# Optimization experiments

Hardware: AMD Instinct MI355X
Metric: run time of the kernel (lower is better)

## Reference

```python
import jax, jax.numpy as jnp
import numpy as np

HIDDEN = 2048
NUM_HEADS = 32
NUM_KV_HEADS = 8
HEAD_DIM = HIDDEN // NUM_HEADS          # 64
Q_PER_KV = NUM_HEADS // NUM_KV_HEADS    # 4
KV_SIZE = HIDDEN * NUM_KV_HEADS // NUM_HEADS  # 512
BATCH, SEQ = 2, 2048


def setup_inputs() -> dict:
    key = jax.random.key(0)
    ks = jax.random.split(key, 10)
    s = 0.02
    return {
        "x": jax.random.normal(ks[0], (BATCH, SEQ, HIDDEN), jnp.float32),
        "attention_mask": jnp.zeros((BATCH, SEQ), jnp.float32),
        "Wq": jax.random.normal(ks[1], (HIDDEN, HIDDEN), jnp.float32) * s,
        "bq": jnp.zeros((HIDDEN,), jnp.float32),
        "Wk": jax.random.normal(ks[2], (HIDDEN, KV_SIZE), jnp.float32) * s,
        "bk": jnp.zeros((KV_SIZE,), jnp.float32),
        "Wv": jax.random.normal(ks[3], (HIDDEN, KV_SIZE), jnp.float32) * s,
        "bv": jnp.zeros((KV_SIZE,), jnp.float32),
        "Wo": jax.random.normal(ks[4], (HIDDEN, HIDDEN), jnp.float32) * s,
        "bo": jnp.zeros((HIDDEN,), jnp.float32),
    }


def reference(x, attention_mask, Wq, bq, Wk, bk, Wv, bv, Wo, bo):
    b, s, _ = x.shape
    q = x @ Wq + bq                                  # [b,s,H]
    k = x @ Wk + bk                                  # [b,s,kv_size]
    v = x @ Wv + bv
    # q -> [b, kv_heads, q_per_kv, s, head_dim]
    q = q.reshape(b, s, NUM_KV_HEADS, Q_PER_KV, HEAD_DIM).transpose(0, 2, 3, 1, 4)
    # k, v -> [b, kv_heads, s, head_dim]
    k = k.reshape(b, s, NUM_KV_HEADS, HEAD_DIM).transpose(0, 2, 1, 3)
    v = v.reshape(b, s, NUM_KV_HEADS, HEAD_DIM).transpose(0, 2, 1, 3)
    scale = 1.0 / jnp.sqrt(jnp.float32(HEAD_DIM))
    scores = jnp.einsum('bhqsd,bhkd->bhqsk', q, k) * scale   # [b,h,qpk,s,s]
    scores = scores + attention_mask.reshape(b, 1, 1, 1, s)
    attn = jax.nn.softmax(scores, axis=-1)
    out = jnp.einsum('bhqsk,bhkd->bhqsd', attn, v)           # [b,h,qpk,s,d]
    out = out.transpose(0, 3, 1, 2, 4).reshape(b, s, HIDDEN)
    return out @ Wo + bo
```

## Files before the change

### kernel.cpp

```cpp
#include <hip/hip_runtime.h>

typedef __attribute__((ext_vector_type(8))) short short8;
typedef __attribute__((ext_vector_type(4))) float floatx4;
typedef __attribute__((ext_vector_type(4))) unsigned int uintx4;

#define B_ 2
#define S_ 2048
#define H_ 2048
#define LOG2E 1.44269504088896f

#define MFMA(a, b, c) __builtin_amdgcn_mfma_f32_16x16x32_bf16(a, b, c, 0, 0, 0)

__device__ __forceinline__ unsigned short f2bf(float f) {
    unsigned int x = __builtin_bit_cast(unsigned int, f);
    unsigned int r = x + 0x7FFFu + ((x >> 16) & 1u);
    return (unsigned short)(r >> 16);
}

__device__ __forceinline__ void gload_lds16(const unsigned short* g, unsigned short* l) {
    __builtin_amdgcn_global_load_lds(
        (const __attribute__((address_space(1))) void*)g,
        (__attribute__((address_space(3))) void*)l, 16, 0, 0);
}

__global__ __launch_bounds__(256) void conv_f2b(const float* __restrict__ in,
                                                unsigned short* __restrict__ out, int n4,
                                                const float* __restrict__ mask,
                                                float* __restrict__ mw) {
    int i = blockIdx.x * 256 + threadIdx.x;
    if (i < n4) {
        float4 v = ((const float4*)in)[i];
        ushort4 o;
        o.x = f2bf(v.x); o.y = f2bf(v.y); o.z = f2bf(v.z); o.w = f2bf(v.w);
        ((ushort4*)out)[i] = o;
    } else {
        for (int m = threadIdx.x; m < B_ * S_; m += 256)
            mw[m] = mask[m] * LOG2E;
    }
}

__global__ __launch_bounds__(256) void tr_f2b(const float* __restrict__ in,
                                              unsigned short* __restrict__ out,
                                              int R, int C) {
    __shared__ unsigned short t[32][33];
    int c0 = blockIdx.x * 32, r0 = blockIdx.y * 32;
    int tx = threadIdx.x & 31, ty = threadIdx.x >> 5;
#pragma unroll
    for (int i = 0; i < 32; i += 8)
        t[ty + i][tx] = f2bf(in[(size_t)(r0 + ty + i) * C + c0 + tx]);
    __syncthreads();
#pragma unroll
    for (int i = 0; i < 32; i += 8)
        out[(size_t)(c0 + ty + i) * R + r0 + tx] = t[tx][ty + i];
}

__global__ __launch_bounds__(256) void tr_wqkv(const float* __restrict__ Wq,
                                               const float* __restrict__ Wk,
                                               const float* __restrict__ Wv,
                                               unsigned short* __restrict__ WqkvT) {
    __shared__ unsigned short t[32][33];
    int bx = blockIdx.x;
    const float* src; int C, c0, orow;
    if (bx < 64)      { src = Wq; C = 2048; c0 = bx * 32;        orow = bx * 32; }
    else if (bx < 80) { src = Wk; C = 512;  c0 = (bx - 64) * 32; orow = 2048 + (bx - 64) * 32; }
    else              { src = Wv; C = 512;  c0 = (bx - 80) * 32; orow = 2560 + (bx - 80) * 32; }
    int r0 = blockIdx.y * 32;
    int tx = threadIdx.x & 31, ty = threadIdx.x >> 5;
#pragma unroll
    for (int i = 0; i < 32; i += 8)
        t[ty + i][tx] = f2bf(src[(size_t)(r0 + ty + i) * C + c0 + tx]);
    __syncthreads();
#pragma unroll
    for (int i = 0; i < 32; i += 8)
        WqkvT[(size_t)(orow + ty + i) * 2048 + r0 + tx] = t[tx][ty + i];
}

__global__ __launch_bounds__(256) void tr_vperm(const unsigned short* __restrict__ in,
                                                unsigned short* __restrict__ out,
                                                int R, int C, int ipitch,
                                                size_t ibs, size_t obs) {
    __shared__ unsigned short t[32][33];
    in += (size_t)blockIdx.z * ibs; out += (size_t)blockIdx.z * obs;
    int c0 = blockIdx.x * 32, r0 = blockIdx.y * 32;
    int tx = threadIdx.x & 31, ty = threadIdx.x >> 5;
#pragma unroll
    for (int i = 0; i < 32; i += 8)
        t[ty + i][tx] = in[(size_t)(r0 + ty + i) * ipitch + c0 + tx];
    __syncthreads();
    int s = r0 + tx;
    int sl = s & 63;
    int j = sl >> 4, q = (sl >> 2) & 3, ii = sl & 3;
    int sp = (s & ~63) + ((j >> 1) << 5) + (q << 3) + ((j & 1) << 2) + ii;
#pragma unroll
    for (int i = 0; i < 32; i += 8)
        out[(size_t)(c0 + ty + i) * R + sp] = t[tx][ty + i];
}

template <bool OUT_F32>
__global__ __launch_bounds__(256) void gemm_bt(const unsigned short* __restrict__ A,
                                               const unsigned short* __restrict__ Bt,
                                               const float* __restrict__ b0,
                                               const float* __restrict__ b1,
                                               const float* __restrict__ b2,
                                               int s1, int s2,
                                               void* __restrict__ Cv,
                                               int M, int N, int K) {
    __shared__ unsigned short As[128 * 64];
    __shared__ unsigned short Bs[128 * 64];
    const int t = threadIdx.x;
    const int lane = t & 63;
    const int wave = t >> 6;
    const int qlane = lane & 15;
    const int quad = lane >> 4;
    const int wm = (wave >> 1) * 64;
    const int wn = (wave & 1) * 64;
    const int bm = blockIdx.y * 128;
    const int bn = blockIdx.x * 128;
    const int srow = t >> 3;
    const int scc = (t & 7) * 8;
    const int gc8 = (((t & 7) ^ (2 * ((t >> 5) & 3))) * 8);
    const int rsw = 2 * (qlane >> 2);

    floatx4 acc[4][4] = {};

    for (int k0 = 0; k0 < K; k0 += 64) {
        __syncthreads();
#pragma unroll
        for (int r = 0; r < 4; ++r) {
            int row = r * 32 + srow;
            gload_lds16(A + (size_t)(bm + row) * K + k0 + gc8, &As[row * 64 + scc]);
        }
#pragma unroll
        for (int r = 0; r < 4; ++r) {
            int row = r * 32 + srow;
            gload_lds16(Bt + (size_t)(bn + row) * K + k0 + gc8, &Bs[row * 64 + scc]);
        }
        __syncthreads();
#pragma unroll
        for (int kk = 0; kk < 2; ++kk) {
            short8 a[4], b[4];
#pragma unroll
            for (int i = 0; i < 4; ++i)
                a[i] = *(const short8*)&As[(wm + i * 16 + qlane) * 64 + ((kk * 4 + quad) ^ rsw) * 8];
#pragma unroll
            for (int j = 0; j < 4; ++j)
                b[j] = *(const short8*)&Bs[(wn + j * 16 + qlane) * 64 + ((kk * 4 + quad) ^ rsw) * 8];
#pragma unroll
            for (int i = 0; i < 4; ++i)
#pragma unroll
                for (int j = 0; j < 4; ++j)
                    acc[i][j] = MFMA(a[i], b[j], acc[i][j]);
        }
    }
#pragma unroll
    for (int j = 0; j < 4; ++j) {
        int col = bn + wn + j * 16 + qlane;
        int cc = col; const float* bp = b0;
        if (col >= s2)      { bp = b2; cc = col - s2; }
        else if (col >= s1) { bp = b1; cc = col - s1; }
        float bvv = bp[cc];
#pragma unroll
        for (int i = 0; i < 4; ++i) {
            int row0 = bm + wm + i * 16 + quad * 4;
#pragma unroll
            for (int r = 0; r < 4; ++r) {
                float v = acc[i][j][r] + bvv;
                if (OUT_F32)
                    ((float*)Cv)[(size_t)(row0 + r) * N + col] = v;
                else
                    ((unsigned short*)Cv)[(size_t)(row0 + r) * N + col] = f2bf(v);
            }
        }
    }
}

__global__ __launch_bounds__(256, 4) void attn_kernel(const unsigned short* __restrict__ qkv,
                                                      const unsigned short* __restrict__ vtb,
                                                      const float* __restrict__ mw,
                                                      unsigned short* __restrict__ ob) {
    const int qt = blockIdx.x;
    const int head = blockIdx.y;
    const int b = blockIdx.z;
    const int kvh = head >> 2;
    const int qcol = head * 64;
    const int kcol = 2048 + kvh * 64;
    const int vch = kvh * 64;
    const int q0 = qt * 128;
    const int t = threadIdx.x;
    const int lane = t & 63;
    const int wave = t >> 6;
    const int qlane = lane & 15;
    const int quad = lane >> 4;
    const int wr = wave * 32;

    __shared__ unsigned short Ks[64 * 64];
    __shared__ unsigned short Vts[2][64 * 64];

    const int gc8 = (((t & 7) ^ (2 * ((t >> 5) & 3))) * 8);
    const int rsw = 2 * (qlane >> 2);
    const float scale2 = 0.125f * LOG2E;

    const unsigned short* vbase = vtb + (size_t)(b * 512 + vch) * S_;
    const float* mbase = mw + (size_t)b * S_;

    short8 aq[2][2];
#pragma unroll
    for (int mi = 0; mi < 2; ++mi)
#pragma unroll
        for (int kk = 0; kk < 2; ++kk)
            aq[mi][kk] = *(const short8*)(qkv +
                (size_t)(b * S_ + q0 + wr + mi * 16 + qlane) * 3072 + qcol + kk * 32 + quad * 8);

    {
        int row = t >> 3;
#pragma unroll
        for (int i = 0; i < 2; ++i) {
            int rr = row + 32 * i;
            gload_lds16(qkv + (size_t)(b * S_ + rr) * 3072 + kcol + gc8,
                        &Ks[(rr * 8 + (t & 7)) * 8]);
            gload_lds16(vbase + (size_t)rr * S_ + gc8,
                        &Vts[0][(rr * 8 + (t & 7)) * 8]);
        }
    }

    short8 ones;
    {
        short v = (qlane == 0) ? (short)0x3F80 : (short)0;
        ones = (short8){v, v, v, v, v, v, v, v};
    }

    floatx4 o[2][4] = {};
    floatx4 osum[2] = {};

    __syncthreads();

    for (int kt = 0; kt < 32; ++kt) {
        const int cur = kt & 1;

        if (kt < 31) {
            const int nxt = cur ^ 1;
            int kn = (kt + 1) * 64;
            int row = t >> 3;
#pragma unroll
            for (int i = 0; i < 2; ++i) {
                int rr = row + 32 * i;
                gload_lds16(vbase + (size_t)rr * S_ + kn + gc8,
                            &Vts[nxt][(rr * 8 + (t & 7)) * 8]);
            }
        }

        unsigned int pk[2][4][2];
#pragma unroll
        for (int jj = 0; jj < 4; jj += 2) {
            floatx4 st[2][2] = {};
            __builtin_amdgcn_s_setprio(1);
#pragma unroll
            for (int dj = 0; dj < 2; ++dj) {
                int j = jj + dj;
                short8 bk0 = *(const short8*)&Ks[(j * 16 + qlane) * 64 + ((0 + quad) ^ rsw) * 8];
                short8 bk1 = *(const short8*)&Ks[(j * 16 + qlane) * 64 + ((4 + quad) ^ rsw) * 8];
#pragma unroll
                for (int mi = 0; mi < 2; ++mi) {
                    st[dj][mi] = MFMA(bk0, aq[mi][0], st[dj][mi]);
                    st[dj][mi] = MFMA(bk1, aq[mi][1], st[dj][mi]);
                }
            }
            __builtin_amdgcn_s_setprio(0);
#pragma unroll
            for (int dj = 0; dj < 2; ++dj) {
                int j = jj + dj;
                floatx4 mv = *(const floatx4*)(mbase + kt * 64 + j * 16 + quad * 4);
#pragma unroll
                for (int mi = 0; mi < 2; ++mi)
#pragma unroll
                    for (int h = 0; h < 2; ++h) {
                        float p0 = __builtin_amdgcn_exp2f(st[dj][mi][2 * h]     * scale2 + mv[2 * h]);
                        float p1 = __builtin_amdgcn_exp2f(st[dj][mi][2 * h + 1] * scale2 + mv[2 * h + 1]);
                        unsigned int r;
                        asm("v_cvt_pk_bf16_f32 %0, %1, %2" : "=v"(r) : "v"(p0), "v"(p1));
                        pk[mi][j][h] = r;
                    }
            }
        }

        __syncthreads();

        if (kt < 31) {
            int kn = (kt + 1) * 64;
            int row = t >> 3;
#pragma unroll
            for (int i = 0; i < 2; ++i) {
                int rr = row + 32 * i;
                gload_lds16(qkv + (size_t)(b * S_ + kn + rr) * 3072 + kcol + gc8,
                            &Ks[(rr * 8 + (t & 7)) * 8]);
            }
        }

        __builtin_amdgcn_s_setprio(1);
#pragma unroll
        for (int kk = 0; kk < 2; ++kk) {
            short8 ap[2];
#pragma unroll
            for (int mi = 0; mi < 2; ++mi) {
                uintx4 u = {pk[mi][2 * kk][0], pk[mi][2 * kk][1],
                            pk[mi][2 * kk + 1][0], pk[mi][2 * kk + 1][1]};
                ap[mi] = __builtin_bit_cast(short8, u);
            }
#pragma unroll
            for (int j2 = 0; j2 < 4; ++j2) {
                short8 bv = *(const short8*)&Vts[cur][(j2 * 16 + qlane) * 64 + ((kk * 4 + quad) ^ rsw) * 8];
#pragma unroll
                for (int mi = 0; mi < 2; ++mi)
                    o[mi][j2] = MFMA(ap[mi], bv, o[mi][j2]);
            }
#pragma unroll
            for (int mi = 0; mi < 2; ++mi)
                osum[mi] = MFMA(ap[mi], ones, osum[mi]);
        }
        __builtin_amdgcn_s_setprio(0);

        __syncthreads();
    }

#pragma unroll
    for (int mi = 0; mi < 2; ++mi)
#pragma unroll
        for (int r = 0; r < 4; ++r) {
            float sm = __shfl(osum[mi][r], quad * 16, 64);
            float inv = 1.0f / sm;
            int row = q0 + wr + mi * 16 + quad * 4 + r;
#pragma unroll
            for (int j2 = 0; j2 < 4; ++j2)
                ob[(size_t)(b * S_ + row) * H_ + qcol + j2 * 16 + qlane] = f2bf(o[mi][j2][r] * inv);
        }
}

extern "C" void kernel_launch(void* const* d_in, const int* in_sizes, int n_in,
                              void* d_out, int out_size, void* d_ws, size_t ws_size,
                              hipStream_t stream) {
    const float* x    = (const float*)d_in[0];
    const float* mask = (const float*)d_in[1];
    const float* Wq   = (const float*)d_in[2];
    const float* bq   = (const float*)d_in[3];
    const float* Wk   = (const float*)d_in[4];
    const float* bk   = (const float*)d_in[5];
    const float* Wv   = (const float*)d_in[6];
    const float* bv   = (const float*)d_in[7];
    const float* Wo   = (const float*)d_in[8];
    const float* bo   = (const float*)d_in[9];
    float* out = (float*)d_out;

    unsigned short* ws = (unsigned short*)d_ws;
    unsigned short* x_bf   = ws;
    unsigned short* qkv    = x_bf + (size_t)4096 * 2048;
    unsigned short* vt_buf = qkv + (size_t)4096 * 3072;
    unsigned short* WqkvT  = vt_buf + (size_t)2 * 512 * 2048;
    unsigned short* WoT    = WqkvT;
    unsigned short* a_buf  = x_bf;

    float* mw = out + (size_t)4096 * 2048 - B_ * S_;

    const int BIG = 1 << 30;
    dim3 blk(256);
    conv_f2b<<<dim3(4096 * 2048 / 4 / 256 + 1), blk, 0, stream>>>(x, x_bf, 4096 * 2048 / 4,
                                                                  mask, mw);
    tr_wqkv<<<dim3(96, 64), blk, 0, stream>>>(Wq, Wk, Wv, WqkvT);
    gemm_bt<false><<<dim3(24, 32), blk, 0, stream>>>(x_bf, WqkvT, bq, bk, bv, 2048, 2560,
                                                     qkv, 4096, 3072, 2048);
    tr_f2b<<<dim3(64, 64), blk, 0, stream>>>(Wo, WoT, 2048, 2048);
    tr_vperm<<<dim3(16, 64, 2), blk, 0, stream>>>(qkv + 2560, vt_buf, 2048, 512, 3072,
                                                  (size_t)2048 * 3072, (size_t)512 * 2048);
    attn_kernel<<<dim3(16, 32, 2), blk, 0, stream>>>(qkv, vt_buf, mw, a_buf);
    gemm_bt<true><<<dim3(16, 32), blk, 0, stream>>>(a_buf, WoT, bo, bo, bo, BIG, BIG,
                                                    out, 4096, 2048, 2048);
}
```

Before: 346.0 us.

## Use 256x256-tile 512-thread GEMM with staged prefetch for QKV projection

Adds a new GEMM kernel with 256x256 output tiles and 8 waves, double-buffered LDS loaded through direct global-to-LDS copies that are interleaved with MFMA phases, plus barriers and s_setprio around the math. It replaces the 128-tile QKV projection GEMM, aiming for more data reuse per loaded tile and overlap of loads with compute. Only 192 blocks are launched on a GPU with many CUs, so the large tile risks leaving CUs underused and raising register pressure.

After: 328.6 us. 1.05x faster.

```diff
diff --git a/kernel.cpp b/kernel.cpp
--- a/kernel.cpp
+++ b/kernel.cpp
@@ -174,6 +174,108 @@
     }
 }
 
+__device__ __forceinline__ void stage_half(const unsigned short* __restrict__ gsrc,
+                                           unsigned short* __restrict__ ldst,
+                                           int t, int K) {
+    const int srow = t >> 3;
+    const int scc = (t & 7) * 8;
+    const int gc8 = (((t & 7) ^ (2 * ((t >> 5) & 3))) * 8);
+#pragma unroll
+    for (int r = 0; r < 2; ++r) {
+        int row = r * 64 + srow;
+        gload_lds16(gsrc + (size_t)row * K + gc8, &ldst[row * 64 + scc]);
+    }
+}
+
+__global__ __launch_bounds__(512) void gemm256(const unsigned short* __restrict__ A,
+                                               const unsigned short* __restrict__ Bt,
+                                               const float* __restrict__ b0,
+                                               const float* __restrict__ b1,
+                                               const float* __restrict__ b2,
+                                               int s1, int s2,
+                                               unsigned short* __restrict__ C,
+                                               int M, int N, int K) {
+    __shared__ unsigned short As[2][256 * 64];
+    __shared__ unsigned short Bs[2][256 * 64];
+    const int t = threadIdx.x;
+    const int lane = t & 63;
+    const int wave = t >> 6;
+    const int qlane = lane & 15;
+    const int quad = lane >> 4;
+    const int wm = (wave >> 2) * 128;
+    const int wn = (wave & 3) * 64;
+    const int bm = blockIdx.y * 256;
+    const int bn = blockIdx.x * 256;
+    const int rsw = 2 * (qlane >> 2);
+
+    floatx4 acc[8][4] = {};
+    const int nt = K / 64;
+
+    stage_half(A  + (size_t)bm * K,         &As[0][0],        t, K);
+    stage_half(A  + (size_t)(bm + 128) * K, &As[0][128 * 64], t, K);
+    stage_half(Bt + (size_t)bn * K,         &Bs[0][0],        t, K);
+    stage_half(Bt + (size_t)(bn + 128) * K, &Bs[0][128 * 64], t, K);
+    __syncthreads();
+
+    for (int i = 0; i < nt; ++i) {
+        const int c = i & 1, nx = c ^ 1;
+        const size_t k1 = (size_t)(i + 1) * 64;
+
+        short8 b[4][2];
+#pragma unroll
+        for (int fc = 0; fc < 4; ++fc)
+#pragma unroll
+            for (int kk = 0; kk < 2; ++kk)
+                b[fc][kk] = *(const short8*)&Bs[c][(wn + fc * 16 + qlane) * 64 + ((kk * 4 + quad) ^ rsw) * 8];
+
+#pragma unroll
+        for (int p = 0; p < 4; ++p) {
+            short8 a[2][2];
+#pragma unroll
+            for (int d = 0; d < 2; ++d)
+#pragma unroll
+                for (int kk = 0; kk < 2; ++kk)
+                    a[d][kk] = *(const short8*)&As[c][(wm + (2 * p + d) * 16 + qlane) * 64 + ((kk * 4 + quad) ^ rsw) * 8];
+
+            if (i + 1 < nt) {
+                if (p == 0) stage_half(A  + (size_t)bm * K + k1,         &As[nx][0],        t, K);
+                if (p == 1) stage_half(A  + (size_t)(bm + 128) * K + k1, &As[nx][128 * 64], t, K);
+                if (p == 2) stage_half(Bt + (size_t)bn * K + k1,         &Bs[nx][0],        t, K);
+                if (p == 3) stage_half(Bt + (size_t)(bn + 128) * K + k1, &Bs[nx][128 * 64], t, K);
+            }
+
+            __builtin_amdgcn_s_barrier();
+            __builtin_amdgcn_s_setprio(1);
+#pragma unroll
+            for (int d = 0; d < 2; ++d)
+#pragma unroll
+                for (int fc = 0; fc < 4; ++fc)
+#pragma unroll
+                    for (int kk = 0; kk < 2; ++kk)
+                        acc[2 * p + d][fc] = MFMA(a[d][kk], b[fc][kk], acc[2 * p + d][fc]);
+            __builtin_amdgcn_s_setprio(0);
+            if (p == 3) asm volatile("s_waitcnt vmcnt(0)" ::: "memory");
+            __builtin_amdgcn_s_barrier();
+        }
+    }
+
+#pragma unroll
+    for (int fc = 0; fc < 4; ++fc) {
+        int col = bn + wn + fc * 16 + qlane;
+        int cc = col; const float* bp = b0;
+        if (col >= s2)      { bp = b2; cc = col - s2; }
+        else if (col >= s1) { bp = b1; cc = col - s1; }
+        float bvv = bp[cc];
+#pragma unroll
+        for (int fr = 0; fr < 8; ++fr) {
+            int row0 = bm + wm + fr * 16 + quad * 4;
+#pragma unroll
+            for (int r = 0; r < 4; ++r)
+                C[(size_t)(row0 + r) * N + col] = f2bf(acc[fr][fc][r] + bvv);
+        }
+    }
+}
+
 __global__ __launch_bounds__(256, 4) void attn_kernel(const unsigned short* __restrict__ qkv,
                                                       const unsigned short* __restrict__ vtb,
                                                       const float* __restrict__ mw,
@@ -365,8 +467,8 @@
     conv_f2b<<<dim3(4096 * 2048 / 4 / 256 + 1), blk, 0, stream>>>(x, x_bf, 4096 * 2048 / 4,
                                                                   mask, mw);
     tr_wqkv<<<dim3(96, 64), blk, 0, stream>>>(Wq, Wk, Wv, WqkvT);
-    gemm_bt<false><<<dim3(24, 32), blk, 0, stream>>>(x_bf, WqkvT, bq, bk, bv, 2048, 2560,
-                                                     qkv, 4096, 3072, 2048);
+    gemm256<<<dim3(12, 16), dim3(512), 0, stream>>>(x_bf, WqkvT, bq, bk, bv, 2048, 2560,
+                                                    qkv, 4096, 3072, 2048);
     tr_f2b<<<dim3(64, 64), blk, 0, stream>>>(Wo, WoT, 2048, 2048);
     tr_vperm<<<dim3(16, 64, 2), blk, 0, stream>>>(qkv + 2560, vt_buf, 2048, 512, 3072,
                                                   (size_t)2048 * 3072, (size_t)512 * 2048);
```
